# Kernel optimization log

Hardware: AMD Instinct MI355X
Metric: run time of the kernel (lower is better)

## Reference

```python
import jax, jax.numpy as jnp
import numpy as np

K = 4096          # num_embeddings
D = 128           # embedding_dim
B = 32768         # flattened batch of latent vectors
COMMIT = 0.25     # commitment_cost


def setup_inputs() -> dict:
    key = jax.random.key(0)
    k_in, k_emb = jax.random.split(key)
    inputs = jax.random.normal(k_in, (B, D), dtype=jnp.float32)
    # buffer init: uniform(-1/K, 1/K) as in the torch module
    embeddings = jax.random.uniform(k_emb, (K, D), dtype=jnp.float32,
                                    minval=-1.0 / K, maxval=1.0 / K)
    return {"inputs": inputs, "embeddings": embeddings}


def reference(inputs, embeddings):
    # eval-mode forward (no EMA buffer update)
    num_embeddings = embeddings.shape[0]
    # squared L2 distances: [B, K]
    distances = (jnp.sum(inputs ** 2, axis=1, keepdims=True)
                 + jnp.sum(embeddings ** 2, axis=1)
                 - 2.0 * inputs @ embeddings.T)
    encoding_indices = jnp.argmin(distances, axis=1)          # [B]
    quantized = embeddings[encoding_indices]                  # [B, D]

    e_latent_loss = jnp.mean((jax.lax.stop_gradient(quantized) - inputs) ** 2)
    # straight-through estimator
    quantized_st = inputs + jax.lax.stop_gradient(quantized - inputs)
    q_latent_loss = jnp.mean((quantized_st - jax.lax.stop_gradient(inputs)) ** 2)
    vq_loss = q_latent_loss + COMMIT * e_latent_loss

    counts = jnp.zeros((num_embeddings,), dtype=jnp.float32).at[encoding_indices].add(1.0)
    avg_probs = counts / inputs.shape[0]
    perplexity = jnp.exp(-jnp.sum(avg_probs * jnp.log(avg_probs + 1e-10)))

    return quantized_st, encoding_indices, vq_loss, e_latent_loss, q_latent_loss, perplexity
```

## Files before the change

### kernel.cpp

```cpp
#include <hip/hip_runtime.h>
#include <math.h>

#define B_ROWS 32768
#define K_CODES 4096
#define D_DIM 128
#define MARGIN 1.5e-3f
#define CAP 64

typedef short bf16x8 __attribute__((ext_vector_type(8)));
typedef float f32x4 __attribute__((ext_vector_type(4)));

__device__ __forceinline__ unsigned short f2bf(float f) {
  union { float f; unsigned int u; } v; v.f = f;
  unsigned int r = (v.u + 0x7FFFu + ((v.u >> 16) & 1u)) >> 16;
  return (unsigned short)r;
}

__global__ __launch_bounds__(256) void prep(const float* __restrict__ x,
                                            const float* __restrict__ emb,
                                            float* __restrict__ x2,
                                            float* __restrict__ e2,
                                            unsigned short* __restrict__ ebb) {
  const int t0 = blockIdx.x * 256 + threadIdx.x;
  const int stride = gridDim.x * 256;
  for (int s = t0; s < B_ROWS * 8; s += stride) {
    int row = s >> 3, lane = s & 7;
    const float* src = x + (size_t)row * D_DIM;
    float v = src[lane];
    float t = v * v;
    asm volatile("" : "+v"(t));
    float acc = t;
#pragma unroll
    for (int i = 1; i < 16; ++i) {
      float w = src[i * 8 + lane];
      float tt = w * w;
      asm volatile("" : "+v"(tt));
      acc = acc + tt;
    }
    acc = acc + __shfl_xor(acc, 1, 64);
    acc = acc + __shfl_xor(acc, 2, 64);
    acc = acc + __shfl_xor(acc, 4, 64);
    if (lane == 0) x2[row] = acc;
  }
  for (int s = t0; s < K_CODES * 8; s += stride) {
    int row = s >> 3, lane = s & 7;
    const float* src = emb + (size_t)row * D_DIM;
    float v = src[lane];
    float t = v * v;
    asm volatile("" : "+v"(t));
    float acc = t;
#pragma unroll
    for (int i = 1; i < 16; ++i) {
      float w = src[i * 8 + lane];
      float tt = w * w;
      asm volatile("" : "+v"(tt));
      acc = acc + tt;
    }
    acc = acc + __shfl_xor(acc, 1, 64);
    acc = acc + __shfl_xor(acc, 2, 64);
    acc = acc + __shfl_xor(acc, 4, 64);
    if (lane == 0) e2[row] = acc;
  }
  for (int og = t0; og < K_CODES * D_DIM / 8; og += stride) {
    int tile = og >> 8, ks = (og >> 6) & 3, qq = (og >> 4) & 3, lr2 = og & 15;
    const float* src = emb + (size_t)(tile * 16 + lr2) * D_DIM + ks * 32 + qq * 8;
    float4 a = *(const float4*)src;
    float4 b = *(const float4*)(src + 4);
    ushort4 o0 = make_ushort4(f2bf(a.x), f2bf(a.y), f2bf(a.z), f2bf(a.w));
    ushort4 o1 = make_ushort4(f2bf(b.x), f2bf(b.y), f2bf(b.z), f2bf(b.w));
    ((ushort4*)ebb)[og * 2] = o0;
    ((ushort4*)ebb)[og * 2 + 1] = o1;
  }
}

__global__ __launch_bounds__(256, 2) void vq_scan(
    const float* __restrict__ x, const unsigned short* __restrict__ eb,
    const float* __restrict__ e2g,
    unsigned short* __restrict__ lists_g, unsigned int* __restrict__ cnt_g) {
  __shared__ float smem[2432];
  unsigned short* lists = (unsigned short*)smem;
  float* m2 = smem + 2048;
  float* mlims = smem + 2304;
  unsigned int* cnt = (unsigned int*)(smem + 2368);

  const int tid = threadIdx.x;
  const int wid = tid >> 6;
  const int lane = tid & 63;
  const int q = lane >> 4, lr = lane & 15;
  const int rowbase = blockIdx.x * 64;
  const bf16x8* ebv = (const bf16x8*)eb;

  bf16x8 af[4][4];
#pragma unroll
  for (int mi = 0; mi < 4; ++mi) {
    const float* xr = x + (size_t)(rowbase + mi * 16 + lr) * D_DIM;
#pragma unroll
    for (int ks = 0; ks < 4; ++ks) {
      float4 v0 = *(const float4*)(xr + ks * 32 + q * 8);
      float4 v1 = *(const float4*)(xr + ks * 32 + q * 8 + 4);
      bf16x8 f;
      f[0] = (short)f2bf(v0.x); f[1] = (short)f2bf(v0.y);
      f[2] = (short)f2bf(v0.z); f[3] = (short)f2bf(v0.w);
      f[4] = (short)f2bf(v1.x); f[5] = (short)f2bf(v1.y);
      f[6] = (short)f2bf(v1.z); f[7] = (short)f2bf(v1.w);
      af[mi][ks] = f;
    }
  }

  float rm[4][4];
#pragma unroll
  for (int mi = 0; mi < 4; ++mi)
#pragma unroll
    for (int rg = 0; rg < 4; ++rg) rm[mi][rg] = 3.4e38f;

#pragma unroll 2
  for (int ch = 0; ch < 32; ++ch) {
    bf16x8 bf[2][4];
#pragma unroll
    for (int ni = 0; ni < 2; ++ni) {
      const bf16x8* tb = ebv + ((size_t)(ch * 8 + wid * 2 + ni) * 256 + lane);
#pragma unroll
      for (int ks = 0; ks < 4; ++ks) bf[ni][ks] = tb[ks * 64];
    }
    f32x4 acc[4][2];
#pragma unroll
    for (int mi = 0; mi < 4; ++mi)
#pragma unroll
      for (int ni = 0; ni < 2; ++ni) {
        f32x4 z = {0.f, 0.f, 0.f, 0.f};
        acc[mi][ni] = z;
      }
#pragma unroll
    for (int ks = 0; ks < 4; ++ks)
#pragma unroll
      for (int mi = 0; mi < 4; ++mi)
#pragma unroll
        for (int ni = 0; ni < 2; ++ni)
          acc[mi][ni] = __builtin_amdgcn_mfma_f32_16x16x32_bf16(
              af[mi][ks], bf[ni][ks], acc[mi][ni], 0, 0, 0);
#pragma unroll
    for (int ni = 0; ni < 2; ++ni) {
      float ev = e2g[ch * 128 + (wid * 2 + ni) * 16 + lr];
#pragma unroll
      for (int mi = 0; mi < 4; ++mi)
#pragma unroll
        for (int rg = 0; rg < 4; ++rg) {
          float t = __builtin_fmaf(-2.0f, acc[mi][ni][rg], ev);
          rm[mi][rg] = fminf(rm[mi][rg], t);
        }
    }
  }

#pragma unroll
  for (int mi = 0; mi < 4; ++mi)
#pragma unroll
    for (int rg = 0; rg < 4; ++rg) {
      float v = rm[mi][rg];
      v = fminf(v, __shfl_xor(v, 1, 64));
      v = fminf(v, __shfl_xor(v, 2, 64));
      v = fminf(v, __shfl_xor(v, 4, 64));
      v = fminf(v, __shfl_xor(v, 8, 64));
      if (lr == 0) m2[(mi * 16 + q * 4 + rg) * 4 + wid] = v;
    }
  __syncthreads();
  if (tid < 64) {
    float a = fminf(m2[tid * 4], m2[tid * 4 + 1]);
    float b = fminf(m2[tid * 4 + 2], m2[tid * 4 + 3]);
    mlims[tid] = fminf(a, b) + MARGIN;
    cnt[tid] = 0;
  }
  __syncthreads();

  float ml[4][4];
#pragma unroll
  for (int mi = 0; mi < 4; ++mi)
#pragma unroll
    for (int rg = 0; rg < 4; ++rg) ml[mi][rg] = mlims[mi * 16 + q * 4 + rg];

#pragma unroll 2
  for (int ch = 0; ch < 32; ++ch) {
    bf16x8 bf[2][4];
#pragma unroll
    for (int ni = 0; ni < 2; ++ni) {
      const bf16x8* tb = ebv + ((size_t)(ch * 8 + wid * 2 + ni) * 256 + lane);
#pragma unroll
      for (int ks = 0; ks < 4; ++ks) bf[ni][ks] = tb[ks * 64];
    }
    f32x4 acc[4][2];
#pragma unroll
    for (int mi = 0; mi < 4; ++mi)
#pragma unroll
      for (int ni = 0; ni < 2; ++ni) {
        f32x4 z = {0.f, 0.f, 0.f, 0.f};
        acc[mi][ni] = z;
      }
#pragma unroll
    for (int ks = 0; ks < 4; ++ks)
#pragma unroll
      for (int mi = 0; mi < 4; ++mi)
#pragma unroll
        for (int ni = 0; ni < 2; ++ni)
          acc[mi][ni] = __builtin_amdgcn_mfma_f32_16x16x32_bf16(
              af[mi][ks], bf[ni][ks], acc[mi][ni], 0, 0, 0);
#pragma unroll
    for (int ni = 0; ni < 2; ++ni) {
      int colbase = ch * 128 + (wid * 2 + ni) * 16 + lr;
      float ev = e2g[colbase];
#pragma unroll
      for (int mi = 0; mi < 4; ++mi)
#pragma unroll
        for (int rg = 0; rg < 4; ++rg) {
          float t = __builtin_fmaf(-2.0f, acc[mi][ni][rg], ev);
          if (t <= ml[mi][rg]) {
            int row = mi * 16 + q * 4 + rg;
            unsigned int p = atomicAdd(&cnt[row], 1u);
            if (p < CAP) lists[row * CAP + p] = (unsigned short)colbase;
          }
        }
    }
  }

  __syncthreads();
#pragma unroll
  for (int p = 0; p < 4; ++p)
    ((ushort4*)(lists_g + (size_t)rowbase * CAP))[p * 256 + tid] =
        ((const ushort4*)lists)[p * 256 + tid];
  if (tid < 64) cnt_g[rowbase + tid] = cnt[tid];
}

__global__ __launch_bounds__(256) void vq_tail2(
    const float* __restrict__ x, const float* __restrict__ emb,
    const float* __restrict__ x2g, const float* __restrict__ e2g,
    const unsigned short* __restrict__ lists_g,
    const unsigned int* __restrict__ cnt_g,
    float* __restrict__ out_q, float* __restrict__ out_idx,
    unsigned int* __restrict__ bidx_g, double* __restrict__ bpart) {
  __shared__ float xf[32 * 132];
  __shared__ float redv[256];
  __shared__ int redi[256];
  __shared__ unsigned int cnts[32];
  __shared__ int bidxs[32];
  __shared__ double lred[8];
  __shared__ int ovflag;

  const int tid = threadIdx.x;
  const int wid = tid >> 6;
  const int lane = tid & 63;
  const int rowbase = blockIdx.x * 32;

  if (tid < 32) cnts[tid] = cnt_g[rowbase + tid];
  {
    const float4* src = (const float4*)(x + (size_t)rowbase * D_DIM);
#pragma unroll
    for (int p = 0; p < 4; ++p) {
      int idx = p * 256 + tid;
      int r = idx >> 5, c = idx & 31;
      *(float4*)(xf + r * 132 + c * 4) = src[idx];
    }
  }
  __syncthreads();

  {
    int gr = tid >> 3, sub = tid & 7;
    int c = (int)cnts[gr];
    if (c <= CAP) {
      float xs2 = x2g[rowbase + gr];
      const float* xr = xf + gr * 132;
      float best = 3.4e38f;
      int bidx = 0x7fffffff;
      const unsigned short* lrow = lists_g + (size_t)(rowbase + gr) * CAP;
      for (int j = sub; j < c; j += 8) {
        int col = lrow[j];
        float dot = 0.f;
        const float4* ev = (const float4*)(emb + (size_t)col * D_DIM);
#pragma unroll 8
        for (int d4 = 0; d4 < 32; ++d4) {
          float4 e4 = ev[d4];
          dot = __builtin_fmaf(xr[d4 * 4 + 0], e4.x, dot);
          dot = __builtin_fmaf(xr[d4 * 4 + 1], e4.y, dot);
          dot = __builtin_fmaf(xr[d4 * 4 + 2], e4.z, dot);
          dot = __builtin_fmaf(xr[d4 * 4 + 3], e4.w, dot);
        }
        float t1 = xs2 + e2g[col];
        float s = __builtin_fmaf(-2.0f, dot, t1);
        if (s < best || (s == best && col < bidx)) { best = s; bidx = col; }
      }
#pragma unroll
      for (int off = 1; off <= 4; off <<= 1) {
        float ov = __shfl_xor(best, off, 64);
        int oi = __shfl_xor(bidx, off, 64);
        if (ov < best || (ov == best && oi < bidx)) { best = ov; bidx = oi; }
      }
      if (sub == 0) {
        out_idx[rowbase + gr] = (float)bidx;
        bidxs[gr] = bidx;
        bidx_g[rowbase + gr] = (unsigned int)bidx;
      }
    }
  }

  if (tid == 0) {
    int f = 0;
    for (int r = 0; r < 32; ++r) f |= (cnts[r] > CAP) ? 1 : 0;
    ovflag = f;
  }
  __syncthreads();

  if (ovflag) {
    for (int r = 0; r < 32; ++r) {
      if (cnts[r] <= CAP) continue;
      float xs2 = x2g[rowbase + r];
      const float* xr = xf + r * 132;
      float lbest = 3.4e38f;
      int lidx = 0x7fffffff;
      for (int c0 = tid; c0 < K_CODES; c0 += 256) {
        float dot = 0.f;
        const float4* ev = (const float4*)(emb + (size_t)c0 * D_DIM);
        for (int d4 = 0; d4 < 32; ++d4) {
          float4 e4 = ev[d4];
          dot = __builtin_fmaf(xr[d4 * 4 + 0], e4.x, dot);
          dot = __builtin_fmaf(xr[d4 * 4 + 1], e4.y, dot);
          dot = __builtin_fmaf(xr[d4 * 4 + 2], e4.z, dot);
          dot = __builtin_fmaf(xr[d4 * 4 + 3], e4.w, dot);
        }
        float s = __builtin_fmaf(-2.0f, dot, xs2 + e2g[c0]);
        if (s < lbest || (s == lbest && c0 < lidx)) { lbest = s; lidx = c0; }
      }
      redv[tid] = lbest;
      redi[tid] = lidx;
      __syncthreads();
      if (tid < 128) {
        float v2 = redv[tid + 128]; int i2 = redi[tid + 128];
        if (v2 < redv[tid] || (v2 == redv[tid] && i2 < redi[tid])) {
          redv[tid] = v2; redi[tid] = i2;
        }
      }
      __syncthreads();
      if (tid < 64) {
        float bv = redv[tid]; int bi = redi[tid];
        float v2 = redv[tid + 64]; int i2 = redi[tid + 64];
        if (v2 < bv || (v2 == bv && i2 < bi)) { bv = v2; bi = i2; }
#pragma unroll
        for (int off = 32; off >= 1; off >>= 1) {
          float ov = __shfl_down(bv, off, 64);
          int oi = __shfl_down(bi, off, 64);
          if (ov < bv || (ov == bv && oi < bi)) { bv = ov; bi = oi; }
        }
        if (tid == 0) {
          out_idx[rowbase + r] = (float)bi;
          bidxs[r] = bi;
          bidx_g[rowbase + r] = (unsigned int)bi;
        }
      }
      __syncthreads();
    }
  }
  __syncthreads();

  {
    int gr = tid >> 3, seg = tid & 7;
    int gidx = bidxs[gr];
    const float4* ev = (const float4*)(emb + (size_t)gidx * D_DIM + seg * 16);
    const float* xvp = xf + gr * 132 + seg * 16;
    float4* oq = (float4*)(out_q + (size_t)(rowbase + gr) * D_DIM + seg * 16);
    double es = 0.0, qs = 0.0;
#pragma unroll
    for (int j = 0; j < 4; ++j) {
      float4 e4 = ev[j];
      float4 xv = *(const float4*)(xvp + j * 4);
      float d0 = e4.x - xv.x, d1 = e4.y - xv.y, d2 = e4.z - xv.z, d3 = e4.w - xv.w;
      float s0 = xv.x + d0, s1 = xv.y + d1, s2 = xv.z + d2, s3 = xv.w + d3;
      oq[j] = make_float4(s0, s1, s2, s3);
      float g0 = s0 - xv.x, g1 = s1 - xv.y, g2 = s2 - xv.z, g3 = s3 - xv.w;
      es += (double)(d0 * d0) + (double)(d1 * d1) + (double)(d2 * d2) + (double)(d3 * d3);
      qs += (double)(g0 * g0) + (double)(g1 * g1) + (double)(g2 * g2) + (double)(g3 * g3);
    }
#pragma unroll
    for (int off = 32; off >= 1; off >>= 1) {
      es += __shfl_down(es, off, 64);
      qs += __shfl_down(qs, off, 64);
    }
    if (lane == 0) { lred[wid * 2] = es; lred[wid * 2 + 1] = qs; }
    __syncthreads();
    if (tid == 0) {
      double e = lred[0] + lred[2] + lred[4] + lred[6];
      double qq = lred[1] + lred[3] + lred[5] + lred[7];
      bpart[(size_t)blockIdx.x * 2] = e;
      bpart[(size_t)blockIdx.x * 2 + 1] = qq;
    }
  }
}

__global__ __launch_bounds__(256) void vq_hist(
    const unsigned int* __restrict__ bidx_g, unsigned int* __restrict__ hist_part) {
  __shared__ unsigned int hist[K_CODES];
  const int tid = threadIdx.x;
#pragma unroll
  for (int i = 0; i < K_CODES / 256; ++i) hist[i * 256 + tid] = 0;
  __syncthreads();
  const int base = blockIdx.x * 512;
#pragma unroll
  for (int i = 0; i < 2; ++i) {
    unsigned int b = bidx_g[base + i * 256 + tid];
    atomicAdd(&hist[b], 1u);
  }
  __syncthreads();
  unsigned int* dst = hist_part + (size_t)blockIdx.x * K_CODES;
#pragma unroll
  for (int i = 0; i < K_CODES / 256; ++i) dst[i * 256 + tid] = hist[i * 256 + tid];
}

__global__ __launch_bounds__(256) void vq_hsum(
    const unsigned int* __restrict__ hist_part, unsigned int* __restrict__ counts) {
  const int k = blockIdx.x * 256 + threadIdx.x;
  unsigned int c = 0;
#pragma unroll 8
  for (int b = 0; b < 64; ++b) c += hist_part[(size_t)b * K_CODES + k];
  counts[k] = c;
}

__global__ __launch_bounds__(256) void vq_final(
    const unsigned int* __restrict__ counts, const double* __restrict__ bpart,
    float* __restrict__ out_scalars) {
  double s = 0.0;
  for (int k = threadIdx.x; k < K_CODES; k += 256) {
    float p = (float)counts[k] * (1.0f / 32768.0f);
    float term = p * logf(p + 1e-10f);
    s += (double)term;
  }
  double e = 0.0, qq = 0.0;
  for (int b = threadIdx.x; b < 1024; b += 256) {
    e += bpart[2 * b];
    qq += bpart[2 * b + 1];
  }
#pragma unroll
  for (int off = 32; off >= 1; off >>= 1) {
    s += __shfl_down(s, off, 64);
    e += __shfl_down(e, off, 64);
    qq += __shfl_down(qq, off, 64);
  }
  __shared__ double red[12];
  if ((threadIdx.x & 63) == 0) {
    int w = threadIdx.x >> 6;
    red[w] = s; red[4 + w] = e; red[8 + w] = qq;
  }
  __syncthreads();
  if (threadIdx.x == 0) {
    double tot = red[0] + red[1] + red[2] + red[3];
    double et = red[4] + red[5] + red[6] + red[7];
    double qt = red[8] + red[9] + red[10] + red[11];
    float e_lat = (float)(et / (double)(B_ROWS * D_DIM));
    float q_lat = (float)(qt / (double)(B_ROWS * D_DIM));
    float vq = q_lat + 0.25f * e_lat;
    out_scalars[0] = vq;
    out_scalars[1] = e_lat;
    out_scalars[2] = q_lat;
    out_scalars[3] = expf(-(float)tot);
  }
}

extern "C" void kernel_launch(void* const* d_in, const int* in_sizes, int n_in,
                              void* d_out, int out_size, void* d_ws, size_t ws_size,
                              hipStream_t stream) {
  const float* x = (const float*)d_in[0];
  const float* emb = (const float*)d_in[1];
  float* out = (float*)d_out;

  double* bpart = (double*)d_ws;
  float* x2 = (float*)((char*)d_ws + 16400);
  float* e2 = (float*)((char*)d_ws + 147472);
  unsigned short* eb = (unsigned short*)((char*)d_ws + 163856);
  unsigned short* lists_g = (unsigned short*)((char*)d_ws + 1212432);
  unsigned int* hist_part = (unsigned int*)((char*)d_ws + 1212432);
  unsigned int* cnt_g = (unsigned int*)((char*)d_ws + 5406736);
  unsigned int* counts = (unsigned int*)((char*)d_ws + 5406736);
  unsigned int* bidx_g = (unsigned int*)((char*)d_ws + 5537808);

  float* out_idx = out + (size_t)B_ROWS * D_DIM;
  float* out_scalars = out_idx + B_ROWS;

  prep<<<512, 256, 0, stream>>>(x, emb, x2, e2, eb);
  vq_scan<<<B_ROWS / 64, 256, 0, stream>>>(x, eb, e2, lists_g, cnt_g);
  vq_tail2<<<B_ROWS / 32, 256, 0, stream>>>(x, emb, x2, e2, lists_g, cnt_g,
                                            out, out_idx, bidx_g, bpart);
  vq_hist<<<64, 256, 0, stream>>>(bidx_g, hist_part);
  vq_hsum<<<K_CODES / 256, 256, 0, stream>>>(hist_part, counts);
  vq_final<<<1, 256, 0, stream>>>(counts, bpart, out_scalars);
}
```

Before: 215.5 us.

## Split vq_scan work across 8 waves with one 16-code tile each

The scan kernel now runs 512 threads per block, and each of the 8 waves handles a single 16-column codebook tile per chunk instead of two. This halves per-wave MFMA work and accumulator registers, and launch bounds ask for 4 blocks per CU to raise occupancy and latency hiding. The cost is that every wave still holds the full A fragments for all 64 rows, so A register pressure and the x loads are duplicated across twice as many waves. The cross-wave min reduction grows to 8 entries.

```diff
diff --git a/kernel.cpp b/kernel.cpp
--- a/kernel.cpp
+++ b/kernel.cpp
@@ -73,15 +73,15 @@
   }
 }
 
-__global__ __launch_bounds__(256, 2) void vq_scan(
+__global__ __launch_bounds__(512, 4) void vq_scan(
     const float* __restrict__ x, const unsigned short* __restrict__ eb,
     const float* __restrict__ e2g,
     unsigned short* __restrict__ lists_g, unsigned int* __restrict__ cnt_g) {
-  __shared__ float smem[2432];
+  __shared__ float smem[2688];
   unsigned short* lists = (unsigned short*)smem;
   float* m2 = smem + 2048;
-  float* mlims = smem + 2304;
-  unsigned int* cnt = (unsigned int*)(smem + 2368);
+  float* mlims = smem + 2560;
+  unsigned int* cnt = (unsigned int*)(smem + 2624);
 
   const int tid = threadIdx.x;
   const int wid = tid >> 6;
@@ -115,40 +115,30 @@
 
 #pragma unroll 2
   for (int ch = 0; ch < 32; ++ch) {
-    bf16x8 bf[2][4];
-#pragma unroll
-    for (int ni = 0; ni < 2; ++ni) {
-      const bf16x8* tb = ebv + ((size_t)(ch * 8 + wid * 2 + ni) * 256 + lane);
-#pragma unroll
-      for (int ks = 0; ks < 4; ++ks) bf[ni][ks] = tb[ks * 64];
-    }
-    f32x4 acc[4][2];
+    const bf16x8* tb = ebv + ((size_t)(ch * 8 + wid) * 256 + lane);
+    bf16x8 bf[4];
+#pragma unroll
+    for (int ks = 0; ks < 4; ++ks) bf[ks] = tb[ks * 64];
+    f32x4 acc[4];
+#pragma unroll
+    for (int mi = 0; mi < 4; ++mi) {
+      f32x4 z = {0.f, 0.f, 0.f, 0.f};
+      acc[mi] = z;
+    }
+#pragma unroll
+    for (int ks = 0; ks < 4; ++ks)
+#pragma unroll
+      for (int mi = 0; mi < 4; ++mi)
+        acc[mi] = __builtin_amdgcn_mfma_f32_16x16x32_bf16(
+            af[mi][ks], bf[ks], acc[mi], 0, 0, 0);
+    float ev = e2g[ch * 128 + wid * 16 + lr];
 #pragma unroll
     for (int mi = 0; mi < 4; ++mi)
 #pragma unroll
-      for (int ni = 0; ni < 2; ++ni) {
-        f32x4 z = {0.f, 0.f, 0.f, 0.f};
-        acc[mi][ni] = z;
-      }
-#pragma unroll
-    for (int ks = 0; ks < 4; ++ks)
-#pragma unroll
-      for (int mi = 0; mi < 4; ++mi)
-#pragma unroll
-        for (int ni = 0; ni < 2; ++ni)
-          acc[mi][ni] = __builtin_amdgcn_mfma_f32_16x16x32_bf16(
-              af[mi][ks], bf[ni][ks], acc[mi][ni], 0, 0, 0);
-#pragma unroll
-    for (int ni = 0; ni < 2; ++ni) {
-      float ev = e2g[ch * 128 + (wid * 2 + ni) * 16 + lr];
-#pragma unroll
-      for (int mi = 0; mi < 4; ++mi)
-#pragma unroll
-        for (int rg = 0; rg < 4; ++rg) {
-          float t = __builtin_fmaf(-2.0f, acc[mi][ni][rg], ev);
-          rm[mi][rg] = fminf(rm[mi][rg], t);
-        }
-    }
+      for (int rg = 0; rg < 4; ++rg) {
+        float t = __builtin_fmaf(-2.0f, acc[mi][rg], ev);
+        rm[mi][rg] = fminf(rm[mi][rg], t);
+      }
   }
 
 #pragma unroll
@@ -160,13 +150,15 @@
       v = fminf(v, __shfl_xor(v, 2, 64));
       v = fminf(v, __shfl_xor(v, 4, 64));
       v = fminf(v, __shfl_xor(v, 8, 64));
-      if (lr == 0) m2[(mi * 16 + q * 4 + rg) * 4 + wid] = v;
+      if (lr == 0) m2[(mi * 16 + q * 4 + rg) * 8 + wid] = v;
     }
   __syncthreads();
   if (tid < 64) {
-    float a = fminf(m2[tid * 4], m2[tid * 4 + 1]);
-    float b = fminf(m2[tid * 4 + 2], m2[tid * 4 + 3]);
-    mlims[tid] = fminf(a, b) + MARGIN;
+    float a = fminf(m2[tid * 8], m2[tid * 8 + 1]);
+    float b = fminf(m2[tid * 8 + 2], m2[tid * 8 + 3]);
+    float c = fminf(m2[tid * 8 + 4], m2[tid * 8 + 5]);
+    float d = fminf(m2[tid * 8 + 6], m2[tid * 8 + 7]);
+    mlims[tid] = fminf(fminf(a, b), fminf(c, d)) + MARGIN;
     cnt[tid] = 0;
   }
   __syncthreads();
@@ -179,52 +171,42 @@
 
 #pragma unroll 2
   for (int ch = 0; ch < 32; ++ch) {
-    bf16x8 bf[2][4];
-#pragma unroll
-    for (int ni = 0; ni < 2; ++ni) {
-      const bf16x8* tb = ebv + ((size_t)(ch * 8 + wid * 2 + ni) * 256 + lane);
-#pragma unroll
-      for (int ks = 0; ks < 4; ++ks) bf[ni][ks] = tb[ks * 64];
-    }
-    f32x4 acc[4][2];
+    const bf16x8* tb = ebv + ((size_t)(ch * 8 + wid) * 256 + lane);
+    bf16x8 bf[4];
+#pragma unroll
+    for (int ks = 0; ks < 4; ++ks) bf[ks] = tb[ks * 64];
+    f32x4 acc[4];
+#pragma unroll
+    for (int mi = 0; mi < 4; ++mi) {
+      f32x4 z = {0.f, 0.f, 0.f, 0.f};
+      acc[mi] = z;
+    }
+#pragma unroll
+    for (int ks = 0; ks < 4; ++ks)
+#pragma unroll
+      for (int mi = 0; mi < 4; ++mi)
+        acc[mi] = __builtin_amdgcn_mfma_f32_16x16x32_bf16(
+            af[mi][ks], bf[ks], acc[mi], 0, 0, 0);
+    int colbase = ch * 128 + wid * 16 + lr;
+    float ev = e2g[colbase];
 #pragma unroll
     for (int mi = 0; mi < 4; ++mi)
 #pragma unroll
-      for (int ni = 0; ni < 2; ++ni) {
-        f32x4 z = {0.f, 0.f, 0.f, 0.f};
-        acc[mi][ni] = z;
-      }
-#pragma unroll
-    for (int ks = 0; ks < 4; ++ks)
-#pragma unroll
-      for (int mi = 0; mi < 4; ++mi)
-#pragma unroll
-        for (int ni = 0; ni < 2; ++ni)
-          acc[mi][ni] = __builtin_amdgcn_mfma_f32_16x16x32_bf16(
-              af[mi][ks], bf[ni][ks], acc[mi][ni], 0, 0, 0);
-#pragma unroll
-    for (int ni = 0; ni < 2; ++ni) {
-      int colbase = ch * 128 + (wid * 2 + ni) * 16 + lr;
-      float ev = e2g[colbase];
-#pragma unroll
-      for (int mi = 0; mi < 4; ++mi)
-#pragma unroll
-        for (int rg = 0; rg < 4; ++rg) {
-          float t = __builtin_fmaf(-2.0f, acc[mi][ni][rg], ev);
-          if (t <= ml[mi][rg]) {
-            int row = mi * 16 + q * 4 + rg;
-            unsigned int p = atomicAdd(&cnt[row], 1u);
-            if (p < CAP) lists[row * CAP + p] = (unsigned short)colbase;
-          }
-        }
-    }
-  }
-
-  __syncthreads();
-#pragma unroll
-  for (int p = 0; p < 4; ++p)
-    ((ushort4*)(lists_g + (size_t)rowbase * CAP))[p * 256 + tid] =
-        ((const ushort4*)lists)[p * 256 + tid];
+      for (int rg = 0; rg < 4; ++rg) {
+        float t = __builtin_fmaf(-2.0f, acc[mi][rg], ev);
+        if (t <= ml[mi][rg]) {
+          int row = mi * 16 + q * 4 + rg;
+          unsigned int p = atomicAdd(&cnt[row], 1u);
+          if (p < CAP) lists[row * CAP + p] = (unsigned short)colbase;
+        }
+      }
+  }
+
+  __syncthreads();
+#pragma unroll
+  for (int p = 0; p < 2; ++p)
+    ((ushort4*)(lists_g + (size_t)rowbase * CAP))[p * 512 + tid] =
+        ((const ushort4*)lists)[p * 512 + tid];
   if (tid < 64) cnt_g[rowbase + tid] = cnt[tid];
 }
 
@@ -480,7 +462,7 @@
   float* out_scalars = out_idx + B_ROWS;
 
   prep<<<512, 256, 0, stream>>>(x, emb, x2, e2, eb);
-  vq_scan<<<B_ROWS / 64, 256, 0, stream>>>(x, eb, e2, lists_g, cnt_g);
+  vq_scan<<<B_ROWS / 64, 512, 0, stream>>>(x, eb, e2, lists_g, cnt_g);
   vq_tail2<<<B_ROWS / 32, 256, 0, stream>>>(x, emb, x2, e2, lists_g, cnt_g,
                                             out, out_idx, bidx_g, bpart);
   vq_hist<<<64, 256, 0, stream>>>(bidx_g, hist_part);
```

Result: slower. 241.8 us (+12.2%).

## Split VQ scan into two-pass kernels over codebook halves with global merge

Applied to the files above, without the earlier changes.

The fused scan kernel is split into a min pass and a candidate-list pass, each launched on twice as many blocks, with every block covering half of the codebook. A small merge kernel combines the two per-row partial minima into thresholds, and candidate lists are appended straight to global memory through global atomics on a counter zeroed by a memset. The goal is more parallelism and better occupancy across the GPU (512 blocks become 1024 per pass). The cost is extra launches, reloading the x fragments in each pass, and global atomics that reorder list entries.

```diff
diff --git a/kernel.cpp b/kernel.cpp
--- a/kernel.cpp
+++ b/kernel.cpp
@@ -73,21 +73,16 @@
   }
 }
 
-__global__ __launch_bounds__(256, 2) void vq_scan(
+__global__ __launch_bounds__(256, 2) void vq_scanA(
     const float* __restrict__ x, const unsigned short* __restrict__ eb,
-    const float* __restrict__ e2g,
-    unsigned short* __restrict__ lists_g, unsigned int* __restrict__ cnt_g) {
-  __shared__ float smem[2432];
-  unsigned short* lists = (unsigned short*)smem;
-  float* m2 = smem + 2048;
-  float* mlims = smem + 2304;
-  unsigned int* cnt = (unsigned int*)(smem + 2368);
-
+    const float* __restrict__ e2g, float* __restrict__ pmin) {
+  __shared__ float m2[256];
   const int tid = threadIdx.x;
   const int wid = tid >> 6;
   const int lane = tid & 63;
   const int q = lane >> 4, lr = lane & 15;
-  const int rowbase = blockIdx.x * 64;
+  const int rg = blockIdx.x >> 1, h = blockIdx.x & 1;
+  const int rowbase = rg * 64;
   const bf16x8* ebv = (const bf16x8*)eb;
 
   bf16x8 af[4][4];
@@ -111,10 +106,11 @@
 #pragma unroll
   for (int mi = 0; mi < 4; ++mi)
 #pragma unroll
-    for (int rg = 0; rg < 4; ++rg) rm[mi][rg] = 3.4e38f;
+    for (int rgi = 0; rgi < 4; ++rgi) rm[mi][rgi] = 3.4e38f;
 
 #pragma unroll 2
-  for (int ch = 0; ch < 32; ++ch) {
+  for (int ch0 = 0; ch0 < 16; ++ch0) {
+    int ch = h * 16 + ch0;
     bf16x8 bf[2][4];
 #pragma unroll
     for (int ni = 0; ni < 2; ++ni) {
@@ -144,9 +140,9 @@
 #pragma unroll
       for (int mi = 0; mi < 4; ++mi)
 #pragma unroll
-        for (int rg = 0; rg < 4; ++rg) {
-          float t = __builtin_fmaf(-2.0f, acc[mi][ni][rg], ev);
-          rm[mi][rg] = fminf(rm[mi][rg], t);
+        for (int rgi = 0; rgi < 4; ++rgi) {
+          float t = __builtin_fmaf(-2.0f, acc[mi][ni][rgi], ev);
+          rm[mi][rgi] = fminf(rm[mi][rgi], t);
         }
     }
   }
@@ -154,31 +150,67 @@
 #pragma unroll
   for (int mi = 0; mi < 4; ++mi)
 #pragma unroll
-    for (int rg = 0; rg < 4; ++rg) {
-      float v = rm[mi][rg];
+    for (int rgi = 0; rgi < 4; ++rgi) {
+      float v = rm[mi][rgi];
       v = fminf(v, __shfl_xor(v, 1, 64));
       v = fminf(v, __shfl_xor(v, 2, 64));
       v = fminf(v, __shfl_xor(v, 4, 64));
       v = fminf(v, __shfl_xor(v, 8, 64));
-      if (lr == 0) m2[(mi * 16 + q * 4 + rg) * 4 + wid] = v;
+      if (lr == 0) m2[(mi * 16 + q * 4 + rgi) * 4 + wid] = v;
     }
   __syncthreads();
   if (tid < 64) {
     float a = fminf(m2[tid * 4], m2[tid * 4 + 1]);
     float b = fminf(m2[tid * 4 + 2], m2[tid * 4 + 3]);
-    mlims[tid] = fminf(a, b) + MARGIN;
-    cnt[tid] = 0;
-  }
-  __syncthreads();
+    pmin[(size_t)(rowbase + tid) * 2 + h] = fminf(a, b);
+  }
+}
+
+__global__ __launch_bounds__(256) void vq_merge(const float* __restrict__ pmin,
+                                               float* __restrict__ mlims) {
+  const int r = blockIdx.x * 256 + threadIdx.x;
+  mlims[r] = fminf(pmin[(size_t)r * 2], pmin[(size_t)r * 2 + 1]) + MARGIN;
+}
+
+__global__ __launch_bounds__(256, 2) void vq_scanB(
+    const float* __restrict__ x, const unsigned short* __restrict__ eb,
+    const float* __restrict__ e2g, const float* __restrict__ mlims,
+    unsigned short* __restrict__ lists_g, unsigned int* __restrict__ cnt_g) {
+  const int tid = threadIdx.x;
+  const int wid = tid >> 6;
+  const int lane = tid & 63;
+  const int q = lane >> 4, lr = lane & 15;
+  const int rg = blockIdx.x >> 1, h = blockIdx.x & 1;
+  const int rowbase = rg * 64;
+  const bf16x8* ebv = (const bf16x8*)eb;
+
+  bf16x8 af[4][4];
+#pragma unroll
+  for (int mi = 0; mi < 4; ++mi) {
+    const float* xr = x + (size_t)(rowbase + mi * 16 + lr) * D_DIM;
+#pragma unroll
+    for (int ks = 0; ks < 4; ++ks) {
+      float4 v0 = *(const float4*)(xr + ks * 32 + q * 8);
+      float4 v1 = *(const float4*)(xr + ks * 32 + q * 8 + 4);
+      bf16x8 f;
+      f[0] = (short)f2bf(v0.x); f[1] = (short)f2bf(v0.y);
+      f[2] = (short)f2bf(v0.z); f[3] = (short)f2bf(v0.w);
+      f[4] = (short)f2bf(v1.x); f[5] = (short)f2bf(v1.y);
+      f[6] = (short)f2bf(v1.z); f[7] = (short)f2bf(v1.w);
+      af[mi][ks] = f;
+    }
+  }
 
   float ml[4][4];
 #pragma unroll
   for (int mi = 0; mi < 4; ++mi)
 #pragma unroll
-    for (int rg = 0; rg < 4; ++rg) ml[mi][rg] = mlims[mi * 16 + q * 4 + rg];
+    for (int rgi = 0; rgi < 4; ++rgi)
+      ml[mi][rgi] = mlims[rowbase + mi * 16 + q * 4 + rgi];
 
 #pragma unroll 2
-  for (int ch = 0; ch < 32; ++ch) {
+  for (int ch0 = 0; ch0 < 16; ++ch0) {
+    int ch = h * 16 + ch0;
     bf16x8 bf[2][4];
 #pragma unroll
     for (int ni = 0; ni < 2; ++ni) {
@@ -209,23 +241,16 @@
 #pragma unroll
       for (int mi = 0; mi < 4; ++mi)
 #pragma unroll
-        for (int rg = 0; rg < 4; ++rg) {
-          float t = __builtin_fmaf(-2.0f, acc[mi][ni][rg], ev);
-          if (t <= ml[mi][rg]) {
-            int row = mi * 16 + q * 4 + rg;
-            unsigned int p = atomicAdd(&cnt[row], 1u);
-            if (p < CAP) lists[row * CAP + p] = (unsigned short)colbase;
+        for (int rgi = 0; rgi < 4; ++rgi) {
+          float t = __builtin_fmaf(-2.0f, acc[mi][ni][rgi], ev);
+          if (t <= ml[mi][rgi]) {
+            int growc = rowbase + mi * 16 + q * 4 + rgi;
+            unsigned int p = atomicAdd(&cnt_g[growc], 1u);
+            if (p < CAP) lists_g[(size_t)growc * CAP + p] = (unsigned short)colbase;
           }
         }
     }
   }
-
-  __syncthreads();
-#pragma unroll
-  for (int p = 0; p < 4; ++p)
-    ((ushort4*)(lists_g + (size_t)rowbase * CAP))[p * 256 + tid] =
-        ((const ushort4*)lists)[p * 256 + tid];
-  if (tid < 64) cnt_g[rowbase + tid] = cnt[tid];
 }
 
 __global__ __launch_bounds__(256) void vq_tail2(
@@ -475,12 +500,17 @@
   unsigned int* cnt_g = (unsigned int*)((char*)d_ws + 5406736);
   unsigned int* counts = (unsigned int*)((char*)d_ws + 5406736);
   unsigned int* bidx_g = (unsigned int*)((char*)d_ws + 5537808);
+  float* pmin = (float*)((char*)d_ws + 5668880);
+  float* mlims = (float*)((char*)d_ws + 5931024);
 
   float* out_idx = out + (size_t)B_ROWS * D_DIM;
   float* out_scalars = out_idx + B_ROWS;
 
+  hipMemsetAsync(cnt_g, 0, 32768 * 4, stream);
   prep<<<512, 256, 0, stream>>>(x, emb, x2, e2, eb);
-  vq_scan<<<B_ROWS / 64, 256, 0, stream>>>(x, eb, e2, lists_g, cnt_g);
+  vq_scanA<<<1024, 256, 0, stream>>>(x, eb, e2, pmin);
+  vq_merge<<<128, 256, 0, stream>>>(pmin, mlims);
+  vq_scanB<<<1024, 256, 0, stream>>>(x, eb, e2, mlims, lists_g, cnt_g);
   vq_tail2<<<B_ROWS / 32, 256, 0, stream>>>(x, emb, x2, e2, lists_g, cnt_g,
                                             out, out_idx, bidx_g, bpart);
   vq_hist<<<64, 256, 0, stream>>>(bidx_g, hist_part);
```

After: 292.7 us. 35.8% more time.

## Double-buffer codebook chunks into LDS via async global_load_lds in both scans

Applied to the files above, without the earlier changes.

Both codebook scan passes in vq_scan now prefetch the next 32 KB bf16 codebook chunk into a double-buffered LDS area with global_load_lds, while the MFMA work for the current chunk runs. Operands are read from LDS, and e2 values are prefetched one chunk ahead. The aim is to hide global-memory latency that previously stalled each chunk's MFMAs. In exchange, LDS use rises to about 64 KB per block, which may lower occupancy below two blocks per CU. The pipeline also relies on hand-written vmcnt waits with no barrier between the LDS write and read; this is safe only because each wave loads and reads its own slice.

```diff
diff --git a/kernel.cpp b/kernel.cpp
--- a/kernel.cpp
+++ b/kernel.cpp
@@ -14,6 +14,12 @@
   union { float f; unsigned int u; } v; v.f = f;
   unsigned int r = (v.u + 0x7FFFu + ((v.u >> 16) & 1u)) >> 16;
   return (unsigned short)r;
+}
+
+__device__ __forceinline__ void gll16(const void* g, void* l) {
+  __builtin_amdgcn_global_load_lds(
+      (const __attribute__((address_space(1))) unsigned int*)g,
+      (__attribute__((address_space(3))) unsigned int*)l, 16, 0, 0);
 }
 
 __global__ __launch_bounds__(256) void prep(const float* __restrict__ x,
@@ -77,18 +83,18 @@
     const float* __restrict__ x, const unsigned short* __restrict__ eb,
     const float* __restrict__ e2g,
     unsigned short* __restrict__ lists_g, unsigned int* __restrict__ cnt_g) {
-  __shared__ float smem[2432];
-  unsigned short* lists = (unsigned short*)smem;
-  float* m2 = smem + 2048;
-  float* mlims = smem + 2304;
-  unsigned int* cnt = (unsigned int*)(smem + 2368);
+  __shared__ bf16x8 ebuf[2][2048];
+  __shared__ unsigned short lists[64 * CAP];
+  __shared__ float m2[256];
+  __shared__ float mlims[64];
+  __shared__ unsigned int cnt[64];
 
   const int tid = threadIdx.x;
   const int wid = tid >> 6;
   const int lane = tid & 63;
   const int q = lane >> 4, lr = lane & 15;
   const int rowbase = blockIdx.x * 64;
-  const bf16x8* ebv = (const bf16x8*)eb;
+  const char* ebB = (const char*)eb;
 
   bf16x8 af[4][4];
 #pragma unroll
@@ -106,6 +112,7 @@
       af[mi][ks] = f;
     }
   }
+  if (tid < 64) cnt[tid] = 0;
 
   float rm[4][4];
 #pragma unroll
@@ -113,41 +120,64 @@
 #pragma unroll
     for (int rg = 0; rg < 4; ++rg) rm[mi][rg] = 3.4e38f;
 
-#pragma unroll 2
-  for (int ch = 0; ch < 32; ++ch) {
-    bf16x8 bf[2][4];
-#pragma unroll
-    for (int ni = 0; ni < 2; ++ni) {
-      const bf16x8* tb = ebv + ((size_t)(ch * 8 + wid * 2 + ni) * 256 + lane);
-#pragma unroll
-      for (int ks = 0; ks < 4; ++ks) bf[ni][ks] = tb[ks * 64];
-    }
-    f32x4 acc[4][2];
-#pragma unroll
-    for (int mi = 0; mi < 4; ++mi)
+  {
+    {
+      const char* src = ebB + wid * 8192 + lane * 16;
+      bf16x8* dst = &ebuf[0][wid * 512];
+#pragma unroll
+      for (int t = 0; t < 8; ++t) gll16(src + t * 1024, (void*)(dst + t * 64));
+    }
+    float evA0 = e2g[(wid * 2) * 16 + lr];
+    float evA1 = e2g[(wid * 2 + 1) * 16 + lr];
+
+#pragma unroll 1
+    for (int ch = 0; ch < 32; ++ch) {
+      float evN0 = 0.f, evN1 = 0.f;
+      if (ch < 31) {
+        const char* src = ebB + (size_t)(ch + 1) * 32768 + wid * 8192 + lane * 16;
+        bf16x8* dst = &ebuf[(ch + 1) & 1][wid * 512];
+#pragma unroll
+        for (int t = 0; t < 8; ++t) gll16(src + t * 1024, (void*)(dst + t * 64));
+        evN0 = e2g[(ch + 1) * 128 + (wid * 2) * 16 + lr];
+        evN1 = e2g[(ch + 1) * 128 + (wid * 2 + 1) * 16 + lr];
+        asm volatile("s_waitcnt vmcnt(10)" ::: "memory");
+      } else {
+        asm volatile("s_waitcnt vmcnt(0)" ::: "memory");
+      }
+      const bf16x8* wb = &ebuf[ch & 1][wid * 512];
+      bf16x8 bf[2][4];
+#pragma unroll
+      for (int ni = 0; ni < 2; ++ni)
+#pragma unroll
+        for (int ks = 0; ks < 4; ++ks) bf[ni][ks] = wb[ni * 256 + ks * 64 + lane];
+      f32x4 acc[4][2];
+#pragma unroll
+      for (int mi = 0; mi < 4; ++mi)
+#pragma unroll
+        for (int ni = 0; ni < 2; ++ni) {
+          f32x4 z = {0.f, 0.f, 0.f, 0.f};
+          acc[mi][ni] = z;
+        }
+#pragma unroll
+      for (int ks = 0; ks < 4; ++ks)
+#pragma unroll
+        for (int mi = 0; mi < 4; ++mi)
+#pragma unroll
+          for (int ni = 0; ni < 2; ++ni)
+            acc[mi][ni] = __builtin_amdgcn_mfma_f32_16x16x32_bf16(
+                af[mi][ks], bf[ni][ks], acc[mi][ni], 0, 0, 0);
 #pragma unroll
       for (int ni = 0; ni < 2; ++ni) {
-        f32x4 z = {0.f, 0.f, 0.f, 0.f};
-        acc[mi][ni] = z;
-      }
-#pragma unroll
-    for (int ks = 0; ks < 4; ++ks)
-#pragma unroll
-      for (int mi = 0; mi < 4; ++mi)
-#pragma unroll
-        for (int ni = 0; ni < 2; ++ni)
-          acc[mi][ni] = __builtin_amdgcn_mfma_f32_16x16x32_bf16(
-              af[mi][ks], bf[ni][ks], acc[mi][ni], 0, 0, 0);
-#pragma unroll
-    for (int ni = 0; ni < 2; ++ni) {
-      float ev = e2g[ch * 128 + (wid * 2 + ni) * 16 + lr];
-#pragma unroll
-      for (int mi = 0; mi < 4; ++mi)
-#pragma unroll
-        for (int rg = 0; rg < 4; ++rg) {
-          float t = __builtin_fmaf(-2.0f, acc[mi][ni][rg], ev);
-          rm[mi][rg] = fminf(rm[mi][rg], t);
-        }
+        float ev = (ni == 0) ? evA0 : evA1;
+#pragma unroll
+        for (int mi = 0; mi < 4; ++mi)
+#pragma unroll
+          for (int rg = 0; rg < 4; ++rg) {
+            float t = __builtin_fmaf(-2.0f, acc[mi][ni][rg], ev);
+            rm[mi][rg] = fminf(rm[mi][rg], t);
+          }
+      }
+      evA0 = evN0; evA1 = evN1;
     }
   }
 
@@ -167,7 +197,6 @@
     float a = fminf(m2[tid * 4], m2[tid * 4 + 1]);
     float b = fminf(m2[tid * 4 + 2], m2[tid * 4 + 3]);
     mlims[tid] = fminf(a, b) + MARGIN;
-    cnt[tid] = 0;
   }
   __syncthreads();
 
@@ -177,46 +206,69 @@
 #pragma unroll
     for (int rg = 0; rg < 4; ++rg) ml[mi][rg] = mlims[mi * 16 + q * 4 + rg];
 
-#pragma unroll 2
-  for (int ch = 0; ch < 32; ++ch) {
-    bf16x8 bf[2][4];
-#pragma unroll
-    for (int ni = 0; ni < 2; ++ni) {
-      const bf16x8* tb = ebv + ((size_t)(ch * 8 + wid * 2 + ni) * 256 + lane);
-#pragma unroll
-      for (int ks = 0; ks < 4; ++ks) bf[ni][ks] = tb[ks * 64];
-    }
-    f32x4 acc[4][2];
-#pragma unroll
-    for (int mi = 0; mi < 4; ++mi)
+  {
+    {
+      const char* src = ebB + wid * 8192 + lane * 16;
+      bf16x8* dst = &ebuf[0][wid * 512];
+#pragma unroll
+      for (int t = 0; t < 8; ++t) gll16(src + t * 1024, (void*)(dst + t * 64));
+    }
+    float evA0 = e2g[(wid * 2) * 16 + lr];
+    float evA1 = e2g[(wid * 2 + 1) * 16 + lr];
+
+#pragma unroll 1
+    for (int ch = 0; ch < 32; ++ch) {
+      float evN0 = 0.f, evN1 = 0.f;
+      if (ch < 31) {
+        const char* src = ebB + (size_t)(ch + 1) * 32768 + wid * 8192 + lane * 16;
+        bf16x8* dst = &ebuf[(ch + 1) & 1][wid * 512];
+#pragma unroll
+        for (int t = 0; t < 8; ++t) gll16(src + t * 1024, (void*)(dst + t * 64));
+        evN0 = e2g[(ch + 1) * 128 + (wid * 2) * 16 + lr];
+        evN1 = e2g[(ch + 1) * 128 + (wid * 2 + 1) * 16 + lr];
+        asm volatile("s_waitcnt vmcnt(10)" ::: "memory");
+      } else {
+        asm volatile("s_waitcnt vmcnt(0)" ::: "memory");
+      }
+      const bf16x8* wb = &ebuf[ch & 1][wid * 512];
+      bf16x8 bf[2][4];
+#pragma unroll
+      for (int ni = 0; ni < 2; ++ni)
+#pragma unroll
+        for (int ks = 0; ks < 4; ++ks) bf[ni][ks] = wb[ni * 256 + ks * 64 + lane];
+      f32x4 acc[4][2];
+#pragma unroll
+      for (int mi = 0; mi < 4; ++mi)
+#pragma unroll
+        for (int ni = 0; ni < 2; ++ni) {
+          f32x4 z = {0.f, 0.f, 0.f, 0.f};
+          acc[mi][ni] = z;
+        }
+#pragma unroll
+      for (int ks = 0; ks < 4; ++ks)
+#pragma unroll
+        for (int mi = 0; mi < 4; ++mi)
+#pragma unroll
+          for (int ni = 0; ni < 2; ++ni)
+            acc[mi][ni] = __builtin_amdgcn_mfma_f32_16x16x32_bf16(
+                af[mi][ks], bf[ni][ks], acc[mi][ni], 0, 0, 0);
 #pragma unroll
       for (int ni = 0; ni < 2; ++ni) {
-        f32x4 z = {0.f, 0.f, 0.f, 0.f};
-        acc[mi][ni] = z;
-      }
-#pragma unroll
-    for (int ks = 0; ks < 4; ++ks)
-#pragma unroll
-      for (int mi = 0; mi < 4; ++mi)
-#pragma unroll
-        for (int ni = 0; ni < 2; ++ni)
-          acc[mi][ni] = __builtin_amdgcn_mfma_f32_16x16x32_bf16(
-              af[mi][ks], bf[ni][ks], acc[mi][ni], 0, 0, 0);
-#pragma unroll
-    for (int ni = 0; ni < 2; ++ni) {
-      int colbase = ch * 128 + (wid * 2 + ni) * 16 + lr;
-      float ev = e2g[colbase];
-#pragma unroll
-      for (int mi = 0; mi < 4; ++mi)
-#pragma unroll
-        for (int rg = 0; rg < 4; ++rg) {
-          float t = __builtin_fmaf(-2.0f, acc[mi][ni][rg], ev);
-          if (t <= ml[mi][rg]) {
-            int row = mi * 16 + q * 4 + rg;
-            unsigned int p = atomicAdd(&cnt[row], 1u);
-            if (p < CAP) lists[row * CAP + p] = (unsigned short)colbase;
+        int colbase = ch * 128 + (wid * 2 + ni) * 16 + lr;
+        float ev = (ni == 0) ? evA0 : evA1;
+#pragma unroll
+        for (int mi = 0; mi < 4; ++mi)
+#pragma unroll
+          for (int rg = 0; rg < 4; ++rg) {
+            float t = __builtin_fmaf(-2.0f, acc[mi][ni][rg], ev);
+            if (t <= ml[mi][rg]) {
+              int row = mi * 16 + q * 4 + rg;
+              unsigned int p = atomicAdd(&cnt[row], 1u);
+              if (p < CAP) lists[row * CAP + p] = (unsigned short)colbase;
+            }
           }
-        }
+      }
+      evA0 = evN0; evA1 = evN1;
     }
   }
 
```

New measurement: 208.2 us. 1.04x faster.
